# Kernel tuning notes

Hardware: AMD Instinct MI355X
Metric: run time of the kernel (lower is better)

Reference implementation:

```python
import jax, jax.numpy as jnp
import numpy as np

ATT_RAW = 312
HID = 900
ATT_DIM = 4096


def setup_inputs() -> dict:
    key = jax.random.key(0)
    ks = jax.random.split(key, 12)
    B, S, N, C = 4, 128, 50, ATT_DIM
    x = jax.random.normal(ks[0], (B, S, C), dtype=jnp.float32)
    x_label = jax.random.randint(ks[1], (B, S), 0, N, dtype=jnp.int64)
    att = jax.random.normal(ks[2], (B, N, ATT_RAW), dtype=jnp.float32)
    att_label = jax.random.randint(ks[3], (B, N), 0, N, dtype=jnp.int64)
    def lin(k, out_f, in_f):
        bound = 1.0 / np.sqrt(in_f)
        kw, kb = jax.random.split(k)
        W = jax.random.uniform(kw, (out_f, in_f), jnp.float32, -bound, bound)
        b = jax.random.uniform(kb, (out_f,), jnp.float32, -bound, bound)
        return W, b
    W1, b1 = lin(ks[4], HID, ATT_RAW)       # attnet layer 1
    W2, b2 = lin(ks[5], ATT_DIM, HID)       # attnet layer 2
    W3, b3 = lin(ks[6], HID, 2 * ATT_DIM)   # o layer 1
    W4, b4 = lin(ks[7], 1, HID)             # o layer 2
    return {"x": x, "x_label": x_label, "att": att, "att_label": att_label,
            "W1": W1, "b1": b1, "W2": W2, "b2": b2,
            "W3": W3, "b3": b3, "W4": W4, "b4": b4}


def reference(x, x_label, att, att_label, W1, b1, W2, b2, W3, b3, W4, b4):
    # x: [B,S,C], att: [B,N,312]; train=True branch -> scalar MSE loss
    B, S, C = x.shape
    N = att.shape[1]
    # attnet: 312 -> 900 -> 4096 with ReLU
    att_f = jax.nn.relu(jax.nn.relu(att @ W1.T + b1) @ W2.T + b2)  # [B,N,4096]
    # o layer 1 on concat([x_f, att_f]) == split matmul + broadcast add
    W3x, W3a = W3[:, :C], W3[:, C:]
    hx = jnp.einsum('bsc,hc->bsh', x, W3x)        # [B,S,900]
    ha = jnp.einsum('bnc,hc->bnh', att_f, W3a)    # [B,N,900]
    pre = jax.nn.relu(hx[:, :, None, :] + ha[:, None, :, :] + b3)  # [B,S,N,900]
    score = jax.nn.sigmoid(jnp.einsum('bsnh,h->bsn', pre, W4[0]) + b4[0])  # [B,S,N]
    label = (x_label[:, :, None] == att_label[:, None, :]).astype(score.dtype)
    loss = jnp.sum((label - score) ** 2) / B / S
    return loss
```

## Files before the change

### kernel.cpp

```cpp
#include <hip/hip_runtime.h>
#include <hip/hip_bf16.h>

typedef __attribute__((ext_vector_type(8))) short bf16x8;
typedef __attribute__((ext_vector_type(4))) float f32x4;
typedef __attribute__((ext_vector_type(8))) unsigned short u16x8;

__device__ __forceinline__ void gload16(const void* g, void* l) {
    __builtin_amdgcn_global_load_lds((const __attribute__((address_space(1))) void*)g,
                                     (__attribute__((address_space(3))) void*)l, 16, 0, 0);
}
__device__ __forceinline__ float bf2f(unsigned short u) {
    union { unsigned i; float f; } v; v.i = ((unsigned)u) << 16; return v.f;
}
__device__ __forceinline__ unsigned short f2bf(float f) {
    __hip_bfloat16 h = __float2bfloat16(f);
    return *(unsigned short*)&h;
}

__device__ __forceinline__ void conv_chunk(
    const float* __restrict__ src, int ld, int col0, int M, int K, int Kp,
    unsigned short* __restrict__ dst, int cid)
{
    const int kp8 = Kp >> 3;
    const int m = cid / kp8;
    const int kc = (cid - m * kp8) << 3;
    u16x8 v;
    if (m < M && kc + 8 <= K) {
        const float* s = src + (size_t)m * ld + col0 + kc;
        const float4 f0 = *(const float4*)s;
        const float4 f1 = *(const float4*)(s + 4);
        const float ff[8] = {f0.x, f0.y, f0.z, f0.w, f1.x, f1.y, f1.z, f1.w};
        #pragma unroll
        for (int j = 0; j < 8; ++j) v[j] = f2bf(ff[j]);
    } else {
        #pragma unroll
        for (int j = 0; j < 8; ++j) {
            float f = 0.f;
            const int k = kc + j;
            if (m < M && k < K) f = src[(size_t)m * ld + col0 + k];
            v[j] = f2bf(f);
        }
    }
    *(u16x8*)(dst + (size_t)m * Kp + kc) = v;
}

template<int ROWS>
__device__ __forceinline__ void stage_f32(
    const float* __restrict__ src, int ld, int row0, int rmax,
    int k0, int kmax, short* __restrict__ lds, int tid)
{
    #pragma unroll
    for (int i = 0; i < ROWS / 32; ++i) {
        const int ch = i * 256 + tid;
        const int r = ch >> 3;
        const int kc8 = (ch & 7) * 8;
        const int gr = row0 + r;
        const int gk = k0 + kc8;
        u16x8 v;
        if (gr < rmax && gk + 8 <= kmax) {
            const float* s = src + (size_t)gr * ld + gk;
            const float4 f0 = *(const float4*)s;
            const float4 f1 = *(const float4*)(s + 4);
            const float ff[8] = {f0.x, f0.y, f0.z, f0.w, f1.x, f1.y, f1.z, f1.w};
            #pragma unroll
            for (int j = 0; j < 8; ++j) v[j] = f2bf(ff[j]);
        } else if (gr < rmax && gk < kmax) {
            #pragma unroll
            for (int j = 0; j < 8; ++j) {
                float f = 0.f;
                if (gk + j < kmax) f = src[(size_t)gr * ld + gk + j];
                v[j] = f2bf(f);
            }
        } else {
            v = (u16x8){0, 0, 0, 0, 0, 0, 0, 0};
        }
        *(u16x8*)((char*)lds + r * 128 + ((kc8 * 2) ^ ((r & 7) << 4))) = v;
    }
}

template<int ROWS>
__device__ __forceinline__ void stage_gl(const unsigned short* __restrict__ src,
                                         int ld, int row0, int k0,
                                         short* __restrict__ lds, int w, int l)
{
    const int sr0 = w * 8 + (l >> 3);
    const int scb = (l & 7) * 16;
    #pragma unroll
    for (int c = 0; c < ROWS / 32; ++c) {
        const int r = c * 32 + sr0;
        const int cbs = scb ^ ((r & 7) << 4);
        const char* g = (const char*)(src + (size_t)(row0 + r) * ld + k0) + cbs;
        char* dst = (char*)lds + (size_t)(c * 32 + w * 8) * 128;
        gload16(g, dst);
    }
}

__device__ __forceinline__ void gemm64_body(
    const unsigned short* __restrict__ A, const unsigned short* __restrict__ B,
    const float* __restrict__ bias, unsigned short* __restrict__ Cout, int ldc,
    int bm, int bn, int Kp, int Mtrue,
    short* As, short* Bs, int tid)
{
    const int w = tid >> 6, l = tid & 63;
    const int wm = w >> 1, wn = w & 1;
    f32x4 acc[2][2];
    #pragma unroll
    for (int i = 0; i < 2; ++i)
        #pragma unroll
        for (int j = 0; j < 2; ++j)
            acc[i][j] = (f32x4){0.f, 0.f, 0.f, 0.f};

    for (int k0 = 0; k0 < Kp; k0 += 64) {
        stage_gl<64>(A, Kp, bm, k0, As, w, l);
        stage_gl<64>(B, Kp, bn, k0, Bs, w, l);
        asm volatile("s_waitcnt vmcnt(0)");
        __syncthreads();
        #pragma unroll
        for (int ks = 0; ks < 64; ks += 32) {
            bf16x8 a[2], b[2];
            const int kb = ks * 2 + (l >> 4) * 16;
            #pragma unroll
            for (int i = 0; i < 2; ++i) {
                const int ra = wm * 32 + i * 16 + (l & 15);
                a[i] = *(const bf16x8*)((const char*)As + ra * 128 + (kb ^ ((ra & 7) << 4)));
                const int rb = wn * 32 + i * 16 + (l & 15);
                b[i] = *(const bf16x8*)((const char*)Bs + rb * 128 + (kb ^ ((rb & 7) << 4)));
            }
            #pragma unroll
            for (int i = 0; i < 2; ++i)
                #pragma unroll
                for (int j = 0; j < 2; ++j)
                    acc[i][j] = __builtin_amdgcn_mfma_f32_16x16x32_bf16(a[i], b[j], acc[i][j], 0, 0, 0);
        }
        __syncthreads();
    }

    #pragma unroll
    for (int i = 0; i < 2; ++i) {
        #pragma unroll
        for (int j = 0; j < 2; ++j) {
            const int col = bn + wn * 32 + j * 16 + (l & 15);
            const float bv = bias[col];
            #pragma unroll
            for (int q = 0; q < 4; ++q) {
                const int row = bm + wm * 32 + i * 16 + (l >> 4) * 4 + q;
                float v = fmaxf(acc[i][j][q] + bv, 0.f);
                if (row >= Mtrue) v = 0.f;
                Cout[(size_t)row * ldc + col] = f2bf(v);
            }
        }
    }
}

__device__ __forceinline__ void gemm128_body(
    const unsigned short* __restrict__ A, const unsigned short* __restrict__ B,
    float* __restrict__ slab, int by, int bx, int k_begin, int k_steps, int Mtrue,
    short* As, short* Bs, int tid)
{
    const int w = tid >> 6, l = tid & 63;
    const int wm = w >> 1, wn = w & 1;
    f32x4 acc[4][4];
    #pragma unroll
    for (int i = 0; i < 4; ++i)
        #pragma unroll
        for (int j = 0; j < 4; ++j)
            acc[i][j] = (f32x4){0.f, 0.f, 0.f, 0.f};

    for (int t = 0; t < k_steps; ++t) {
        const int k0 = k_begin + t * 64;
        stage_gl<128>(A, 4096, by * 128, k0, As, w, l);
        stage_gl<128>(B, 4096, bx * 128, k0, Bs, w, l);
        asm volatile("s_waitcnt vmcnt(0)");
        __syncthreads();
        #pragma unroll
        for (int ks = 0; ks < 64; ks += 32) {
            bf16x8 a[4], b[4];
            const int kb = ks * 2 + (l >> 4) * 16;
            #pragma unroll
            for (int i = 0; i < 4; ++i) {
                const int ra = wm * 64 + i * 16 + (l & 15);
                a[i] = *(const bf16x8*)((const char*)As + ra * 128 + (kb ^ ((ra & 7) << 4)));
                const int rb = wn * 64 + i * 16 + (l & 15);
                b[i] = *(const bf16x8*)((const char*)Bs + rb * 128 + (kb ^ ((rb & 7) << 4)));
            }
            #pragma unroll
            for (int i = 0; i < 4; ++i)
                #pragma unroll
                for (int j = 0; j < 4; ++j)
                    acc[i][j] = __builtin_amdgcn_mfma_f32_16x16x32_bf16(a[i], b[j], acc[i][j], 0, 0, 0);
        }
        __syncthreads();
    }

    #pragma unroll
    for (int i = 0; i < 4; ++i) {
        #pragma unroll
        for (int j = 0; j < 4; ++j) {
            const int col = bx * 128 + wn * 64 + j * 16 + (l & 15);
            if (col >= 900) continue;
            #pragma unroll
            for (int q = 0; q < 4; ++q) {
                const int row = by * 128 + wm * 64 + i * 16 + (l >> 4) * 4 + q;
                if (row < Mtrue)
                    slab[(size_t)row * 900 + col] = acc[i][j][q];
            }
        }
    }
}

template<int NS>
__device__ __forceinline__ void reduceNS(const float* __restrict__ p,
                                         const float* __restrict__ bias,
                                         unsigned short* __restrict__ o,
                                         int M, int idx)
{
    const int m = idx / 113;
    const int c = idx - m * 113;
    const int k = c * 8;
    u16x8 v;
    #pragma unroll
    for (int q = 0; q < 8; q += 4) {
        if (k + q < 900) {
            float4 a = *(const float4*)(p + (size_t)m * 900 + k + q);
            #pragma unroll 1
            for (int s = 1; s < NS; ++s) {
                const float4 t = *(const float4*)(p + ((size_t)s * M + m) * 900 + k + q);
                a.x += t.x; a.y += t.y; a.z += t.z; a.w += t.w;
            }
            if (bias) {
                const float4 bb = *(const float4*)(bias + k + q);
                a.x += bb.x; a.y += bb.y; a.z += bb.z; a.w += bb.w;
            }
            v[q + 0] = f2bf(a.x); v[q + 1] = f2bf(a.y);
            v[q + 2] = f2bf(a.z); v[q + 3] = f2bf(a.w);
        } else {
            #pragma unroll
            for (int j = 0; j < 4; ++j) v[q + j] = 0;
        }
    }
    *(u16x8*)(o + (size_t)m * 904 + k) = v;
}

struct PadJob {
    const float* src; unsigned short* dst;
    int src_ld, col0, M, K, Kp;
    int chunk_begin;
};
struct PG1Args {
    PadJob j[3]; int total;
    const float *att, *W1, *b1;
    unsigned short* h1;
    float* out;
};

__global__ __launch_bounds__(256)
void padg1(PG1Args P)
{
    __shared__ short As[64 * 64];
    __shared__ short Bs[64 * 64];
    const int gid = blockIdx.x;
    const int tid = threadIdx.x;

    if (gid < 60) {
        const int bm = (gid & 3) * 64, bn = (gid >> 2) * 64;
        const int w = tid >> 6, l = tid & 63;
        const int wm = w >> 1, wn = w & 1;

        f32x4 acc[2][2];
        #pragma unroll
        for (int i = 0; i < 2; ++i)
            #pragma unroll
            for (int j = 0; j < 2; ++j)
                acc[i][j] = (f32x4){0.f, 0.f, 0.f, 0.f};

        for (int k0 = 0; k0 < 320; k0 += 64) {
            stage_f32<64>(P.att, 312, bm, 200, k0, 312, As, tid);
            stage_f32<64>(P.W1,  312, bn, 900, k0, 312, Bs, tid);
            __syncthreads();
            #pragma unroll
            for (int ks = 0; ks < 64; ks += 32) {
                bf16x8 a[2], b[2];
                const int kb = ks * 2 + (l >> 4) * 16;
                #pragma unroll
                for (int i = 0; i < 2; ++i) {
                    const int ra = wm * 32 + i * 16 + (l & 15);
                    a[i] = *(const bf16x8*)((const char*)As + ra * 128 + (kb ^ ((ra & 7) << 4)));
                    const int rb = wn * 32 + i * 16 + (l & 15);
                    b[i] = *(const bf16x8*)((const char*)Bs + rb * 128 + (kb ^ ((rb & 7) << 4)));
                }
                #pragma unroll
                for (int i = 0; i < 2; ++i)
                    #pragma unroll
                    for (int j = 0; j < 2; ++j)
                        acc[i][j] = __builtin_amdgcn_mfma_f32_16x16x32_bf16(a[i], b[j], acc[i][j], 0, 0, 0);
            }
            __syncthreads();
        }

        #pragma unroll
        for (int i = 0; i < 2; ++i) {
            #pragma unroll
            for (int j = 0; j < 2; ++j) {
                const int col = bn + wn * 32 + j * 16 + (l & 15);
                const float bv = (col < 900) ? P.b1[col] : 0.f;
                #pragma unroll
                for (int q = 0; q < 4; ++q) {
                    const int row = bm + wm * 32 + i * 16 + (l >> 4) * 4 + q;
                    float v = fmaxf(acc[i][j][q] + bv, 0.f);
                    if (row >= 200) v = 0.f;
                    P.h1[(size_t)row * 960 + col] = f2bf(v);
                }
            }
        }
        return;
    }

    if (gid == 60 && tid == 0) P.out[0] = 0.f;

    const int idx = (gid - 60) * 256 + tid;
    if (idx >= P.total) return;
    int ji = 0;
    #pragma unroll
    for (int k = 1; k < 3; ++k) if (idx >= P.j[k].chunk_begin) ji = k;
    const PadJob J = P.j[ji];
    conv_chunk(J.src, J.src_ld, J.col0, J.M, J.K, J.Kp, J.dst, idx - J.chunk_begin);
}

struct L2Args {
    const unsigned short *xb, *W3xb; float* hxp;
    const unsigned short *h1, *W2b; const float* b2; unsigned short* attf;
    const float* W3; unsigned short* W3a_bf;
};

__global__ __launch_bounds__(256)
void g23w(L2Args a)
{
    __shared__ short As[128 * 64];
    __shared__ short Bs[128 * 64];
    const int gid = blockIdx.x;
    const int tid = threadIdx.x;

    if (gid < 256) {
        const int z = gid >> 5, by = (gid >> 3) & 3, bx = gid & 7;
        gemm128_body(a.xb, a.W3xb, a.hxp + (size_t)z * 512 * 900,
                     by, bx, z * 512, 8, 512, As, Bs, tid);
    } else if (gid < 512) {
        const int g = gid - 256;
        gemm64_body(a.h1, a.W2b, a.b2, a.attf, 4096,
                    (g >> 6) * 64, (g & 63) * 64, 960, 200, As, Bs, tid);
    } else {
        conv_chunk(a.W3, 8192, 4096, 900, 4096, 4096, a.W3a_bf, (gid - 512) * 256 + tid);
    }
}

struct L3Args {
    const unsigned short *attf, *W3ab; float* hap;
    const float *hxp, *b3; unsigned short* hx_bf;
};

__global__ __launch_bounds__(256)
void g4r(L3Args a)
{
    __shared__ short As[128 * 64];
    __shared__ short Bs[128 * 64];
    const int gid = blockIdx.x;
    const int tid = threadIdx.x;

    if (gid < 256) {
        const int z = gid >> 4, by = (gid >> 3) & 1, bx = gid & 7;
        gemm128_body(a.attf, a.W3ab, a.hap + (size_t)z * 200 * 900,
                     by, bx, z * 256, 4, 200, As, Bs, tid);
    } else {
        const int idx = (gid - 256) * 256 + tid;
        if (idx < 57856) reduceNS<8>(a.hxp, a.b3, a.hx_bf, 512, idx);
    }
}

__global__ __launch_bounds__(256)
void red_ha(const float* __restrict__ hap, unsigned short* __restrict__ ha_bf)
{
    const int idx = blockIdx.x * 256 + threadIdx.x;
    if (idx < 22600) reduceNS<16>(hap, nullptr, ha_bf, 200, idx);
}

__global__ __launch_bounds__(512)
void score_loss(const unsigned short* __restrict__ hxb,
                const unsigned short* __restrict__ hab,
                const float* __restrict__ W4,
                const float* __restrict__ b4,
                const int* __restrict__ xl,
                const int* __restrict__ al,
                float* __restrict__ out)
{
    __shared__ __align__(16) unsigned short hxs[8 * 904];
    __shared__ __align__(16) unsigned short has[16 * 904];
    __shared__ __align__(16) float w4s[904];
    __shared__ float zpart[4][8][16];
    __shared__ float red[2];

    const int tid = threadIdx.x;
    const int nt = blockIdx.x, st = blockIdx.y, b = blockIdx.z;
    const int row0 = b * 128 + st * 8;

    for (int t = tid; t < 24 * 113; t += 512) {
        u16x8 v;
        unsigned short* dst;
        if (t < 8 * 113) {
            const int r = t / 113, c = t - r * 113;
            v = *(const u16x8*)(hxb + (size_t)(row0 + r) * 904 + c * 8);
            dst = hxs + r * 904 + c * 8;
        } else {
            const int t2 = t - 8 * 113;
            const int r = t2 / 113, c = t2 - r * 113;
            const int n = nt * 16 + r;
            if (n < 50) v = *(const u16x8*)(hab + (size_t)(b * 50 + n) * 904 + c * 8);
            else        v = (u16x8){0,0,0,0,0,0,0,0};
            dst = has + r * 904 + c * 8;
        }
        *(u16x8*)dst = v;
    }
    for (int t = tid; t < 226; t += 512) {
        float4 v = {0.f, 0.f, 0.f, 0.f};
        if (t < 225) v = *(const float4*)(W4 + t * 4);
        *(float4*)(w4s + t * 4) = v;
    }
    __syncthreads();

    const int hs = tid >> 7;
    const int si = (tid >> 4) & 7;
    const int ni = tid & 15;

    float acc = 0.f;
    const unsigned short* hrow = hxs + si * 904;
    const unsigned short* arow = has + ni * 904;
    for (int c = hs; c < 113; c += 4) {
        const u16x8 hv = *(const u16x8*)(hrow + c * 8);
        const u16x8 av = *(const u16x8*)(arow + c * 8);
        const float4 w0 = *(const float4*)(w4s + c * 8);
        const float4 w1 = *(const float4*)(w4s + c * 8 + 4);
        const float ww[8] = {w0.x, w0.y, w0.z, w0.w, w1.x, w1.y, w1.z, w1.w};
        #pragma unroll
        for (int j = 0; j < 8; ++j) {
            const float u = bf2f((unsigned short)hv[j]) + bf2f((unsigned short)av[j]);
            acc = fmaf(fmaxf(u, 0.f), ww[j], acc);
        }
    }
    zpart[hs][si][ni] = acc;
    __syncthreads();

    float dd = 0.f;
    if (tid < 128) {
        const int esi = tid >> 4, eni = tid & 15;
        const int n = nt * 16 + eni;
        const float z = zpart[0][esi][eni] + zpart[1][esi][eni]
                      + zpart[2][esi][eni] + zpart[3][esi][eni] + b4[0];
        const float sc = 1.f / (1.f + __expf(-z));
        if (n < 50) {
            const float lab = (xl[row0 + esi] == al[b * 50 + n]) ? 1.f : 0.f;
            const float d = lab - sc;
            dd = d * d;
        }
        #pragma unroll
        for (int off = 32; off > 0; off >>= 1)
            dd += __shfl_down(dd, off);
        if ((tid & 63) == 0) red[tid >> 6] = dd;
    }
    __syncthreads();
    if (tid == 0)
        atomicAdd(out, (red[0] + red[1]) * (1.f / 512.f));
}

extern "C" void kernel_launch(void* const* d_in, const int* in_sizes, int n_in,
                              void* d_out, int out_size, void* d_ws, size_t ws_size,
                              hipStream_t stream)
{
    const float* x   = (const float*)d_in[0];
    const int*   xl  = (const int*)  d_in[1];
    const float* att = (const float*)d_in[2];
    const int*   al  = (const int*)  d_in[3];
    const float* W1  = (const float*)d_in[4];
    const float* b1  = (const float*)d_in[5];
    const float* W2  = (const float*)d_in[6];
    const float* b2  = (const float*)d_in[7];
    const float* W3  = (const float*)d_in[8];
    const float* b3  = (const float*)d_in[9];
    const float* W4  = (const float*)d_in[10];
    const float* b4  = (const float*)d_in[11];
    float* out = (float*)d_out;

    const int B = 4, S = 128, N = 50, C = 4096, H = 900, AR = 312;
    const int MS = B * S;
    const int MN = B * N;
    const int MNp = 256;
    const int Hp = 960;
    const int W3p = 1024;

    char* base = (char*)d_ws;
    size_t off = 0;
    auto alloc = [&](size_t bytes) { void* r = base + off; off = (off + bytes + 255) & ~(size_t)255; return r; };
    unsigned short* x_bf   = (unsigned short*)alloc((size_t)MS * C * 2);
    unsigned short* W2_bf  = (unsigned short*)alloc((size_t)C * Hp * 2);
    unsigned short* W3x_bf = (unsigned short*)alloc((size_t)W3p * C * 2);
    unsigned short* W3a_bf = (unsigned short*)alloc((size_t)W3p * C * 2);
    unsigned short* h1_bf  = (unsigned short*)alloc((size_t)MNp * Hp * 2);
    unsigned short* attf_bf= (unsigned short*)alloc((size_t)MNp * C * 2);
    float* hxp = (float*)alloc((size_t)8 * MS * H * 4);
    float* hap = (float*)alloc((size_t)16 * MN * H * 4);
    unsigned short* hx_bf = (unsigned short*)alloc((size_t)MS * 904 * 2);
    unsigned short* ha_bf = (unsigned short*)alloc((size_t)MN * 904 * 2);

    const dim3 blk(256);
    auto cdiv = [](int a, int b) { return (a + b - 1) / b; };

    PG1Args P;
    int cb = 0;
    auto setjob = [&](int i, const float* src, unsigned short* dst, int ld, int col0,
                      int M, int K, int Kp, int Mp) {
        P.j[i] = PadJob{src, dst, ld, col0, M, K, Kp, cb};
        cb += Mp * (Kp >> 3);
    };
    setjob(0, x,   x_bf,   C,     0, MS, C,  C,   MS);
    setjob(1, W2,  W2_bf,  H,     0, C,  H,  Hp,  C);
    setjob(2, W3,  W3x_bf, 2 * C, 0, H,  C,  C,   W3p);
    P.total = cb;
    P.att = att; P.W1 = W1; P.b1 = b1; P.h1 = h1_bf; P.out = out;
    padg1<<<dim3(60 + cdiv(cb, 256)), blk, 0, stream>>>(P);

    L2Args A2{x_bf, W3x_bf, hxp, h1_bf, W2_bf, b2, attf_bf, W3, W3a_bf};
    g23w<<<dim3(2560), blk, 0, stream>>>(A2);

    L3Args A3{attf_bf, W3a_bf, hap, hxp, b3, hx_bf};
    g4r<<<dim3(482), blk, 0, stream>>>(A3);

    red_ha<<<dim3(cdiv(MN * 113, 256)), blk, 0, stream>>>(hap, ha_bf);

    score_loss<<<dim3(4, 16, 4), dim3(512), 0, stream>>>(hx_bf, ha_bf, W4, b4, xl, al, out);
}
```

Baseline: 70.38 us.

## Fold ha split-K reduction into score kernel and move W3a conversion earlier

```diff
diff --git a/kernel.cpp b/kernel.cpp
--- a/kernel.cpp
+++ b/kernel.cpp
@@ -247,7 +247,7 @@
     int chunk_begin;
 };
 struct PG1Args {
-    PadJob j[3]; int total;
+    PadJob j[4]; int total;
     const float *att, *W1, *b1;
     unsigned short* h1;
     float* out;
@@ -321,7 +321,7 @@
     if (idx >= P.total) return;
     int ji = 0;
     #pragma unroll
-    for (int k = 1; k < 3; ++k) if (idx >= P.j[k].chunk_begin) ji = k;
+    for (int k = 1; k < 4; ++k) if (idx >= P.j[k].chunk_begin) ji = k;
     const PadJob J = P.j[ji];
     conv_chunk(J.src, J.src_ld, J.col0, J.M, J.K, J.Kp, J.dst, idx - J.chunk_begin);
 }
@@ -329,11 +329,10 @@
 struct L2Args {
     const unsigned short *xb, *W3xb; float* hxp;
     const unsigned short *h1, *W2b; const float* b2; unsigned short* attf;
-    const float* W3; unsigned short* W3a_bf;
 };
 
 __global__ __launch_bounds__(256)
-void g23w(L2Args a)
+void g23(L2Args a)
 {
     __shared__ short As[128 * 64];
     __shared__ short Bs[128 * 64];
@@ -344,12 +343,10 @@
         const int z = gid >> 5, by = (gid >> 3) & 3, bx = gid & 7;
         gemm128_body(a.xb, a.W3xb, a.hxp + (size_t)z * 512 * 900,
                      by, bx, z * 512, 8, 512, As, Bs, tid);
-    } else if (gid < 512) {
+    } else {
         const int g = gid - 256;
         gemm64_body(a.h1, a.W2b, a.b2, a.attf, 4096,
                     (g >> 6) * 64, (g & 63) * 64, 960, 200, As, Bs, tid);
-    } else {
-        conv_chunk(a.W3, 8192, 4096, 900, 4096, 4096, a.W3a_bf, (gid - 512) * 256 + tid);
     }
 }
 
@@ -366,26 +363,19 @@
     const int gid = blockIdx.x;
     const int tid = threadIdx.x;
 
-    if (gid < 256) {
+    if (gid < 128) {
         const int z = gid >> 4, by = (gid >> 3) & 1, bx = gid & 7;
         gemm128_body(a.attf, a.W3ab, a.hap + (size_t)z * 200 * 900,
-                     by, bx, z * 256, 4, 200, As, Bs, tid);
+                     by, bx, z * 512, 8, 200, As, Bs, tid);
     } else {
-        const int idx = (gid - 256) * 256 + tid;
+        const int idx = (gid - 128) * 256 + tid;
         if (idx < 57856) reduceNS<8>(a.hxp, a.b3, a.hx_bf, 512, idx);
     }
-}
-
-__global__ __launch_bounds__(256)
-void red_ha(const float* __restrict__ hap, unsigned short* __restrict__ ha_bf)
-{
-    const int idx = blockIdx.x * 256 + threadIdx.x;
-    if (idx < 22600) reduceNS<16>(hap, nullptr, ha_bf, 200, idx);
 }
 
 __global__ __launch_bounds__(512)
 void score_loss(const unsigned short* __restrict__ hxb,
-                const unsigned short* __restrict__ hab,
+                const float* __restrict__ hap,
                 const float* __restrict__ W4,
                 const float* __restrict__ b4,
                 const int* __restrict__ xl,
@@ -412,10 +402,26 @@
         } else {
             const int t2 = t - 8 * 113;
             const int r = t2 / 113, c = t2 - r * 113;
+            const int k = c * 8;
             const int n = nt * 16 + r;
-            if (n < 50) v = *(const u16x8*)(hab + (size_t)(b * 50 + n) * 904 + c * 8);
-            else        v = (u16x8){0,0,0,0,0,0,0,0};
-            dst = has + r * 904 + c * 8;
+            float f[8] = {0.f, 0.f, 0.f, 0.f, 0.f, 0.f, 0.f, 0.f};
+            if (n < 50) {
+                const int row = b * 50 + n;
+                #pragma unroll
+                for (int q = 0; q < 8; q += 4) {
+                    if (k + q < 900) {
+                        #pragma unroll 1
+                        for (int s = 0; s < 8; ++s) {
+                            const float4 a0 = *(const float4*)(hap + ((size_t)s * 200 + row) * 900 + k + q);
+                            f[q + 0] += a0.x; f[q + 1] += a0.y;
+                            f[q + 2] += a0.z; f[q + 3] += a0.w;
+                        }
+                    }
+                }
+            }
+            #pragma unroll
+            for (int j = 0; j < 8; ++j) v[j] = f2bf(f[j]);
+            dst = has + r * 904 + k;
         }
         *(u16x8*)dst = v;
     }
@@ -505,9 +511,8 @@
     unsigned short* h1_bf  = (unsigned short*)alloc((size_t)MNp * Hp * 2);
     unsigned short* attf_bf= (unsigned short*)alloc((size_t)MNp * C * 2);
     float* hxp = (float*)alloc((size_t)8 * MS * H * 4);
-    float* hap = (float*)alloc((size_t)16 * MN * H * 4);
+    float* hap = (float*)alloc((size_t)8 * MN * H * 4);
     unsigned short* hx_bf = (unsigned short*)alloc((size_t)MS * 904 * 2);
-    unsigned short* ha_bf = (unsigned short*)alloc((size_t)MN * 904 * 2);
 
     const dim3 blk(256);
     auto cdiv = [](int a, int b) { return (a + b - 1) / b; };
@@ -522,17 +527,16 @@
     setjob(0, x,   x_bf,   C,     0, MS, C,  C,   MS);
     setjob(1, W2,  W2_bf,  H,     0, C,  H,  Hp,  C);
     setjob(2, W3,  W3x_bf, 2 * C, 0, H,  C,  C,   W3p);
+    setjob(3, W3,  W3a_bf, 2 * C, C, H,  C,  C,   W3p);
     P.total = cb;
     P.att = att; P.W1 = W1; P.b1 = b1; P.h1 = h1_bf; P.out = out;
     padg1<<<dim3(60 + cdiv(cb, 256)), blk, 0, stream>>>(P);
 
-    L2Args A2{x_bf, W3x_bf, hxp, h1_bf, W2_bf, b2, attf_bf, W3, W3a_bf};
-    g23w<<<dim3(2560), blk, 0, stream>>>(A2);
+    L2Args A2{x_bf, W3x_bf, hxp, h1_bf, W2_bf, b2, attf_bf};
+    g23<<<dim3(512), blk, 0, stream>>>(A2);
 
     L3Args A3{attf_bf, W3a_bf, hap, hxp, b3, hx_bf};
-    g4r<<<dim3(482), blk, 0, stream>>>(A3);
-
-    red_ha<<<dim3(cdiv(MN * 113, 256)), blk, 0, stream>>>(hap, ha_bf);
-
-    score_loss<<<dim3(4, 16, 4), dim3(512), 0, stream>>>(hx_bf, ha_bf, W4, b4, xl, al, out);
-}
+    g4r<<<dim3(354), blk, 0, stream>>>(A3);
+
+    score_loss<<<dim3(4, 16, 4), dim3(512), 0, stream>>>(hx_bf, hap, W4, b4, xl, al, out);
+}
```

Result: slower. 73.20 us (+4.0%).
